# Kernel optimization log

Hardware: AMD Instinct MI355X
Metric: run time of the kernel (lower is better)

The kernel has to match this reference:

```python
import jax, jax.numpy as jnp
from jax import lax
import numpy as np

B, N, D = 8, 4096, 64
S = 1024          # groups
K = 32            # kneighbors
RADIUS = 0.2


def farthest_point_sample(xyz, npoint):
    """xyz: [B,N,3] -> centroid indices [B,npoint]. Deterministic start at index 0
    (original torch uses a random start index)."""
    b, n, _ = xyz.shape

    def step(carry, _):
        distance, farthest = carry                              # [B,N], [B]
        centroid = jnp.take_along_axis(xyz, farthest[:, None, None], axis=1)  # [B,1,3]
        dist = jnp.sum((xyz - centroid) ** 2, axis=-1)          # [B,N]
        distance = jnp.minimum(distance, dist)
        new_far = jnp.argmax(distance, axis=-1)
        return (distance, new_far), farthest

    init = (jnp.full((b, n), 1e10, xyz.dtype), jnp.zeros((b,), jnp.int32))
    _, cents = lax.scan(step, init, None, length=npoint)        # [npoint,B]
    return cents.T                                              # [B,npoint]


def square_distance(src, dst):
    # [B,N,M] squared euclidean distances
    d = -2.0 * jnp.einsum('bnc,bmc->bnm', src, dst)
    d += jnp.sum(src ** 2, -1)[:, :, None]
    d += jnp.sum(dst ** 2, -1)[:, None, :]
    return d


def query_ball_point(radius, nsample, xyz, new_xyz):
    b, n, _ = xyz.shape
    s = new_xyz.shape[1]
    sqrdists = square_distance(new_xyz, xyz)                    # [B,S,N]
    arange = jnp.arange(n, dtype=jnp.int32)[None, None, :]
    group_idx = jnp.where(sqrdists > radius ** 2, n, arange)    # [B,S,N]
    group_idx = jnp.sort(group_idx, axis=-1)[:, :, :nsample]    # [B,S,K]
    first = group_idx[:, :, :1]
    group_idx = jnp.where(group_idx == n, first, group_idx)
    return group_idx


def gather_points(points, idx):
    # points [B,N,C], idx [B,...] -> [B,...,C]
    return jax.vmap(lambda p, i: p[i])(points, idx)


def setup_inputs() -> dict:
    key = jax.random.key(0)
    k1, k2 = jax.random.split(key)
    xyz = jax.random.uniform(k1, (B, N, 3), dtype=jnp.float32)
    points = jax.random.normal(k2, (B, N, D), dtype=jnp.float32)
    return {"xyz": xyz, "points": points}


def reference(xyz, points):
    fps_idx = farthest_point_sample(xyz, S)                     # [B,S]
    new_xyz = gather_points(xyz, fps_idx)                       # [B,S,3]
    anchor_feat = gather_points(points, fps_idx)                # [B,S,D]
    idx = query_ball_point(RADIUS, K, xyz, new_xyz)             # [B,S,K]
    grouped_xyz = gather_points(xyz, idx)                       # [B,S,K,3]
    grouped_points = gather_points(points, idx)                 # [B,S,K,D]
    grouped_points = jnp.concatenate([grouped_points, grouped_xyz], axis=-1)  # use_xyz
    anchor_rep = jnp.broadcast_to(anchor_feat[:, :, None, :], (B, S, K, D))
    new_points = jnp.concatenate([grouped_points, anchor_rep], axis=-1)  # [B,S,K,2D+3]
    return new_xyz, new_points
```

## Files before the change

### kernel.cpp

```cpp
#include <hip/hip_runtime.h>

#define BB 8
#define NN 4096
#define DD 64
#define SS 1024
#define KK 32
#define R2 0.04f
#define NCONS_BLK 248
#define NCONS_WAVE (NCONS_BLK * 8)

typedef float f32x2 __attribute__((ext_vector_type(2)));

#define DPP_MAXF(wv, CTRL)                                                             \
    {                                                                                  \
        int _o = __builtin_amdgcn_update_dpp(__float_as_int(wv), __float_as_int(wv),   \
                                             CTRL, 0xf, 0xf, false);                   \
        (wv) = fmaxf((wv), __int_as_float(_o));                                        \
    }

__global__ __launch_bounds__(512) void fused_kernel(const float* __restrict__ xyz,
                                                    const float* __restrict__ points,
                                                    float* __restrict__ out,
                                                    int* __restrict__ fps_g,
                                                    int* __restrict__ progress) {
#pragma clang fp contract(off)
    __shared__ float4 sxyz[NN];
    __shared__ unsigned long long red[SS];
    __shared__ int sfar[SS];
    __shared__ int bbuf[8][KK];

    const int tid  = threadIdx.x;
    const int wave = tid >> 6;
    const int lane = tid & 63;

    if (blockIdx.x < BB) {
        const int b = blockIdx.x;
        const float* xb = xyz + (size_t)b * NN * 3;

        for (int i = tid; i < SS; i += 512) red[i] = 0ull;

        const float4* xb4 = (const float4*)(xb + tid * 24);
        const float4 q0 = xb4[0], q1 = xb4[1], q2 = xb4[2];
        const float4 q3 = xb4[3], q4 = xb4[4], q5 = xb4[5];

        f32x2 px[4], py[4], pz[4], dist[4];
        px[0] = (f32x2){q0.x, q0.w}; py[0] = (f32x2){q0.y, q1.x}; pz[0] = (f32x2){q0.z, q1.y};
        px[1] = (f32x2){q1.z, q2.y}; py[1] = (f32x2){q1.w, q2.z}; pz[1] = (f32x2){q2.x, q2.w};
        px[2] = (f32x2){q3.x, q3.w}; py[2] = (f32x2){q3.y, q4.x}; pz[2] = (f32x2){q3.z, q4.y};
        px[3] = (f32x2){q4.z, q5.y}; py[3] = (f32x2){q4.w, q5.z}; pz[3] = (f32x2){q5.x, q5.w};
#pragma unroll
        for (int jj = 0; jj < 4; ++jj) {
            const int i0 = tid * 8 + 2 * jj;
            sxyz[i0]     = make_float4(px[jj].x, py[jj].x, pz[jj].x, 0.0f);
            sxyz[i0 + 1] = make_float4(px[jj].y, py[jj].y, pz[jj].y, 0.0f);
            dist[jj] = (f32x2){1e10f, 1e10f};
        }
        __syncthreads();

        int far = 0;
        for (int t = 0; t < SS; ++t) {
            if (tid == 0) sfar[t] = far;
            const float4 c = sxyz[far];
            const f32x2 cx2 = (f32x2){c.x, c.x}, cy2 = (f32x2){c.y, c.y},
                        cz2 = (f32x2){c.z, c.z};

            f32x2 nd[4];
#pragma unroll
            for (int jj = 0; jj < 4; ++jj) {
                const f32x2 dx = px[jj] - cx2;
                const f32x2 dy = py[jj] - cy2;
                const f32x2 dz = pz[jj] - cz2;
                const f32x2 d  = (dx * dx + dy * dy) + dz * dz;
                f32x2 m;
                m.x = fminf(dist[jj].x, d.x);
                m.y = fminf(dist[jj].y, d.y);
                dist[jj] = m;
                nd[jj] = m;
            }
            const float bestv =
                fmaxf(fmaxf(fmaxf(nd[0].x, nd[0].y), fmaxf(nd[1].x, nd[1].y)),
                      fmaxf(fmaxf(nd[2].x, nd[2].y), fmaxf(nd[3].x, nd[3].y)));
            int localj = 0;
#pragma unroll
            for (int j = 7; j >= 0; --j) {
                const float v = (j & 1) ? nd[j >> 1].y : nd[j >> 1].x;
                if (v == bestv) localj = j;
            }

            float wv = bestv;
            DPP_MAXF(wv, 0x111);
            DPP_MAXF(wv, 0x112);
            DPP_MAXF(wv, 0x114);
            DPP_MAXF(wv, 0x118);
            DPP_MAXF(wv, 0x142);
            DPP_MAXF(wv, 0x143);
            const float maxw =
                __int_as_float(__builtin_amdgcn_readlane(__float_as_int(wv), 63));

            const unsigned long long hits = __ballot(bestv == maxw);
            const int L = __ffsll(hits) - 1;
            const int candv = tid * 8 + localj;
            const int cand  = __builtin_amdgcn_readlane(candv, L);

            if (lane == 0) {
                const unsigned long long p =
                    ((unsigned long long)__float_as_uint(maxw) << 32) | (unsigned)(~cand);
                atomicMax(&red[t], p);
            }
            __syncthreads();
            far = (int)(~(unsigned)red[t]);

            if ((t & 31) == 31 && wave == 7) {
                const int c0 = t - 31;
                if (lane < 32) fps_g[b * SS + c0 + lane] = sfar[c0 + lane];
                __threadfence();
                if (lane == 0)
                    __hip_atomic_store(&progress[b], t + 1, __ATOMIC_RELEASE,
                                       __HIP_MEMORY_SCOPE_AGENT);
            }
        }
    } else {
        const int wid = (blockIdx.x - BB) * 8 + wave;
        for (int g = wid; g < BB * SS; g += NCONS_WAVE) {
            const int b = g >> 10;
            const int s = g & (SS - 1);
            while (__hip_atomic_load(&progress[b], __ATOMIC_ACQUIRE,
                                     __HIP_MEMORY_SCOPE_AGENT) <= s)
                __builtin_amdgcn_s_sleep(32);
            const int qi = __hip_atomic_load(&fps_g[g], __ATOMIC_RELAXED,
                                             __HIP_MEMORY_SCOPE_AGENT);

            const float* xb = xyz + (size_t)b * NN * 3;
            const float* pb = points + (size_t)b * NN * DD;
            const float qx = xb[qi * 3 + 0], qy = xb[qi * 3 + 1], qz = xb[qi * 3 + 2];
            const float qn = __fadd_rn(__fadd_rn(__fmul_rn(qx, qx), __fmul_rn(qy, qy)),
                                       __fmul_rn(qz, qz));

            int total = 0;
            for (int base = 0; base < NN && total < KK; base += 64) {
                const int n  = base + lane;
                const float px = xb[n * 3 + 0], py = xb[n * 3 + 1], pz = xb[n * 3 + 2];
                const float pn = __fadd_rn(__fadd_rn(__fmul_rn(px, px), __fmul_rn(py, py)),
                                           __fmul_rn(pz, pz));
                const float dt = __fadd_rn(__fadd_rn(__fmul_rn(qx, px), __fmul_rn(qy, py)),
                                           __fmul_rn(qz, pz));
                const float d = __fadd_rn(__fadd_rn(__fmul_rn(-2.0f, dt), qn), pn);
                const bool hit = !(d > R2);
                const unsigned long long mask = __ballot(hit);
                const int before = __popcll(mask & ((1ull << lane) - 1ull));
                const int pos = total + before;
                if (hit && pos < KK) bbuf[wave][pos] = n;
                total += (int)__popcll(mask);
            }
            if (lane < KK) {
                const int v = (lane < total) ? bbuf[wave][lane] : bbuf[wave][0];
                bbuf[wave][lane] = v;
            }

            if (lane < 3) out[(size_t)g * 3 + lane] = xb[qi * 3 + lane];

            float* outp = out + (size_t)BB * SS * 3 + (size_t)g * (KK * 131);
            for (int c = lane; c < KK * 131; c += 64) {
                const int k = c / 131;
                const int j = c - k * 131;
                const int idx = bbuf[wave][k];
                float v;
                if (j < DD)          v = pb[idx * DD + j];
                else if (j < DD + 3) v = xb[idx * 3 + (j - DD)];
                else                 v = pb[qi * DD + (j - DD - 3)];
                outp[c] = v;
            }
        }
    }
}

extern "C" void kernel_launch(void* const* d_in, const int* in_sizes, int n_in,
                              void* d_out, int out_size, void* d_ws, size_t ws_size,
                              hipStream_t stream) {
    const float* xyz    = (const float*)d_in[0];
    const float* points = (const float*)d_in[1];
    float* out = (float*)d_out;

    int* fps_g    = (int*)d_ws;
    int* progress = fps_g + BB * SS;

    fused_kernel<<<BB + NCONS_BLK, 512, 0, stream>>>(xyz, points, out, fps_g, progress);
}
```

Before: 810.5 us.

## Replicate FPS per block and drop producer-consumer progress synchronization

The kernel now launches 32 blocks per batch. Every block recomputes the full farthest-point sampling for its batch and then groups its own slice of 32 centroids, reading coordinates from shared memory. This removes the global-memory progress flags, fences and spin-waiting between 8 producer blocks and many consumer blocks. The gather loop is also restructured so each lane writes one feature per neighbor. In exchange, the ball query and output writes no longer overlap with FPS; they run as a tail after it, and FPS work is duplicated 32 times. The padded shared array appears meant to keep one block per CU.

```diff
diff --git a/kernel.cpp b/kernel.cpp
--- a/kernel.cpp
+++ b/kernel.cpp
@@ -6,8 +6,6 @@
 #define SS 1024
 #define KK 32
 #define R2 0.04f
-#define NCONS_BLK 248
-#define NCONS_WAVE (NCONS_BLK * 8)
 
 typedef float f32x2 __attribute__((ext_vector_type(2)));
 
@@ -20,156 +18,142 @@
 
 __global__ __launch_bounds__(512) void fused_kernel(const float* __restrict__ xyz,
                                                     const float* __restrict__ points,
-                                                    float* __restrict__ out,
-                                                    int* __restrict__ fps_g,
-                                                    int* __restrict__ progress) {
+                                                    float* __restrict__ out) {
 #pragma clang fp contract(off)
     __shared__ float4 sxyz[NN];
-    __shared__ unsigned long long red[SS];
+    __shared__ unsigned long long red[SS + 416];
     __shared__ int sfar[SS];
     __shared__ int bbuf[8][KK];
 
     const int tid  = threadIdx.x;
     const int wave = tid >> 6;
     const int lane = tid & 63;
+    const int b    = blockIdx.x >> 5;
+    const int cs   = blockIdx.x & 31;
+    const float* xb = xyz + (size_t)b * NN * 3;
+    const float* pb = points + (size_t)b * NN * DD;
 
-    if (blockIdx.x < BB) {
-        const int b = blockIdx.x;
-        const float* xb = xyz + (size_t)b * NN * 3;
+    for (int i = tid; i < SS; i += 512) red[i] = 0ull;
 
-        for (int i = tid; i < SS; i += 512) red[i] = 0ull;
+    const float4* xb4 = (const float4*)(xb + tid * 24);
+    const float4 q0 = xb4[0], q1 = xb4[1], q2 = xb4[2];
+    const float4 q3 = xb4[3], q4 = xb4[4], q5 = xb4[5];
 
-        const float4* xb4 = (const float4*)(xb + tid * 24);
-        const float4 q0 = xb4[0], q1 = xb4[1], q2 = xb4[2];
-        const float4 q3 = xb4[3], q4 = xb4[4], q5 = xb4[5];
+    f32x2 px[4], py[4], pz[4], dist[4];
+    px[0] = (f32x2){q0.x, q0.w}; py[0] = (f32x2){q0.y, q1.x}; pz[0] = (f32x2){q0.z, q1.y};
+    px[1] = (f32x2){q1.z, q2.y}; py[1] = (f32x2){q1.w, q2.z}; pz[1] = (f32x2){q2.x, q2.w};
+    px[2] = (f32x2){q3.x, q3.w}; py[2] = (f32x2){q3.y, q4.x}; pz[2] = (f32x2){q3.z, q4.y};
+    px[3] = (f32x2){q4.z, q5.y}; py[3] = (f32x2){q4.w, q5.z}; pz[3] = (f32x2){q5.x, q5.w};
+#pragma unroll
+    for (int jj = 0; jj < 4; ++jj) {
+        const int i0 = tid * 8 + 2 * jj;
+        sxyz[i0]     = make_float4(px[jj].x, py[jj].x, pz[jj].x, 0.0f);
+        sxyz[i0 + 1] = make_float4(px[jj].y, py[jj].y, pz[jj].y, 0.0f);
+        dist[jj] = (f32x2){1e10f, 1e10f};
+    }
+    __syncthreads();
 
-        f32x2 px[4], py[4], pz[4], dist[4];
-        px[0] = (f32x2){q0.x, q0.w}; py[0] = (f32x2){q0.y, q1.x}; pz[0] = (f32x2){q0.z, q1.y};
-        px[1] = (f32x2){q1.z, q2.y}; py[1] = (f32x2){q1.w, q2.z}; pz[1] = (f32x2){q2.x, q2.w};
-        px[2] = (f32x2){q3.x, q3.w}; py[2] = (f32x2){q3.y, q4.x}; pz[2] = (f32x2){q3.z, q4.y};
-        px[3] = (f32x2){q4.z, q5.y}; py[3] = (f32x2){q4.w, q5.z}; pz[3] = (f32x2){q5.x, q5.w};
+    int far = 0;
+    for (int t = 0; t < SS; ++t) {
+        if (tid == 0) sfar[t] = far;
+        const float4 c = sxyz[far];
+        const f32x2 cx2 = (f32x2){c.x, c.x}, cy2 = (f32x2){c.y, c.y},
+                    cz2 = (f32x2){c.z, c.z};
+
+        f32x2 nd[4];
 #pragma unroll
         for (int jj = 0; jj < 4; ++jj) {
-            const int i0 = tid * 8 + 2 * jj;
-            sxyz[i0]     = make_float4(px[jj].x, py[jj].x, pz[jj].x, 0.0f);
-            sxyz[i0 + 1] = make_float4(px[jj].y, py[jj].y, pz[jj].y, 0.0f);
-            dist[jj] = (f32x2){1e10f, 1e10f};
+            const f32x2 dx = px[jj] - cx2;
+            const f32x2 dy = py[jj] - cy2;
+            const f32x2 dz = pz[jj] - cz2;
+            const f32x2 d  = (dx * dx + dy * dy) + dz * dz;
+            f32x2 m;
+            m.x = fminf(dist[jj].x, d.x);
+            m.y = fminf(dist[jj].y, d.y);
+            dist[jj] = m;
+            nd[jj] = m;
+        }
+        const float bestv =
+            fmaxf(fmaxf(fmaxf(nd[0].x, nd[0].y), fmaxf(nd[1].x, nd[1].y)),
+                  fmaxf(fmaxf(nd[2].x, nd[2].y), fmaxf(nd[3].x, nd[3].y)));
+        int localj = 0;
+#pragma unroll
+        for (int j = 7; j >= 0; --j) {
+            const float v = (j & 1) ? nd[j >> 1].y : nd[j >> 1].x;
+            if (v == bestv) localj = j;
+        }
+
+        float wv = bestv;
+        DPP_MAXF(wv, 0x111);
+        DPP_MAXF(wv, 0x112);
+        DPP_MAXF(wv, 0x114);
+        DPP_MAXF(wv, 0x118);
+        DPP_MAXF(wv, 0x142);
+        DPP_MAXF(wv, 0x143);
+        const float maxw =
+            __int_as_float(__builtin_amdgcn_readlane(__float_as_int(wv), 63));
+
+        const unsigned long long hits = __ballot(bestv == maxw);
+        const int L = __ffsll(hits) - 1;
+        const int candv = tid * 8 + localj;
+        const int cand  = __builtin_amdgcn_readlane(candv, L);
+
+        if (lane == 0) {
+            const unsigned long long p =
+                ((unsigned long long)__float_as_uint(maxw) << 32) | (unsigned)(~cand);
+            atomicMax(&red[t], p);
         }
         __syncthreads();
+        far = (int)(~(unsigned)red[t]);
+    }
 
-        int far = 0;
-        for (int t = 0; t < SS; ++t) {
-            if (tid == 0) sfar[t] = far;
-            const float4 c = sxyz[far];
-            const f32x2 cx2 = (f32x2){c.x, c.x}, cy2 = (f32x2){c.y, c.y},
-                        cz2 = (f32x2){c.z, c.z};
+#pragma unroll
+    for (int i = 0; i < 4; ++i) {
+        const int s  = cs * 32 + wave * 4 + i;
+        const int g  = b * SS + s;
+        const int qi = sfar[s];
+        const float4 q = sxyz[qi];
+        const float qn = __fadd_rn(__fadd_rn(__fmul_rn(q.x, q.x), __fmul_rn(q.y, q.y)),
+                                   __fmul_rn(q.z, q.z));
 
-            f32x2 nd[4];
-#pragma unroll
-            for (int jj = 0; jj < 4; ++jj) {
-                const f32x2 dx = px[jj] - cx2;
-                const f32x2 dy = py[jj] - cy2;
-                const f32x2 dz = pz[jj] - cz2;
-                const f32x2 d  = (dx * dx + dy * dy) + dz * dz;
-                f32x2 m;
-                m.x = fminf(dist[jj].x, d.x);
-                m.y = fminf(dist[jj].y, d.y);
-                dist[jj] = m;
-                nd[jj] = m;
-            }
-            const float bestv =
-                fmaxf(fmaxf(fmaxf(nd[0].x, nd[0].y), fmaxf(nd[1].x, nd[1].y)),
-                      fmaxf(fmaxf(nd[2].x, nd[2].y), fmaxf(nd[3].x, nd[3].y)));
-            int localj = 0;
-#pragma unroll
-            for (int j = 7; j >= 0; --j) {
-                const float v = (j & 1) ? nd[j >> 1].y : nd[j >> 1].x;
-                if (v == bestv) localj = j;
-            }
+        int total = 0;
+        for (int base = 0; base < NN && total < KK; base += 64) {
+            const int n = base + lane;
+            const float4 p = sxyz[n];
+            const float pn = __fadd_rn(__fadd_rn(__fmul_rn(p.x, p.x), __fmul_rn(p.y, p.y)),
+                                       __fmul_rn(p.z, p.z));
+            const float dt = __fadd_rn(__fadd_rn(__fmul_rn(q.x, p.x), __fmul_rn(q.y, p.y)),
+                                       __fmul_rn(q.z, p.z));
+            const float d = __fadd_rn(__fadd_rn(__fmul_rn(-2.0f, dt), qn), pn);
+            const bool hit = !(d > R2);
+            const unsigned long long mask = __ballot(hit);
+            const int before = __popcll(mask & ((1ull << lane) - 1ull));
+            const int pos = total + before;
+            if (hit && pos < KK) bbuf[wave][pos] = n;
+            total += (int)__popcll(mask);
+        }
+        if (lane < KK) {
+            const int v = (lane < total) ? bbuf[wave][lane] : bbuf[wave][0];
+            bbuf[wave][lane] = v;
+        }
 
-            float wv = bestv;
-            DPP_MAXF(wv, 0x111);
-            DPP_MAXF(wv, 0x112);
-            DPP_MAXF(wv, 0x114);
-            DPP_MAXF(wv, 0x118);
-            DPP_MAXF(wv, 0x142);
-            DPP_MAXF(wv, 0x143);
-            const float maxw =
-                __int_as_float(__builtin_amdgcn_readlane(__float_as_int(wv), 63));
+        if (lane < 3)
+            out[(size_t)g * 3 + lane] = (lane == 0) ? q.x : (lane == 1) ? q.y : q.z;
 
-            const unsigned long long hits = __ballot(bestv == maxw);
-            const int L = __ffsll(hits) - 1;
-            const int candv = tid * 8 + localj;
-            const int cand  = __builtin_amdgcn_readlane(candv, L);
+        const float a1 = (lane >= 3) ? pb[qi * DD + (lane - 3)] : 0.0f;
+        const float a2 = (lane < 3) ? pb[qi * DD + (61 + lane)] : 0.0f;
 
-            if (lane == 0) {
-                const unsigned long long p =
-                    ((unsigned long long)__float_as_uint(maxw) << 32) | (unsigned)(~cand);
-                atomicMax(&red[t], p);
-            }
-            __syncthreads();
-            far = (int)(~(unsigned)red[t]);
-
-            if ((t & 31) == 31 && wave == 7) {
-                const int c0 = t - 31;
-                if (lane < 32) fps_g[b * SS + c0 + lane] = sfar[c0 + lane];
-                __threadfence();
-                if (lane == 0)
-                    __hip_atomic_store(&progress[b], t + 1, __ATOMIC_RELEASE,
-                                       __HIP_MEMORY_SCOPE_AGENT);
-            }
-        }
-    } else {
-        const int wid = (blockIdx.x - BB) * 8 + wave;
-        for (int g = wid; g < BB * SS; g += NCONS_WAVE) {
-            const int b = g >> 10;
-            const int s = g & (SS - 1);
-            while (__hip_atomic_load(&progress[b], __ATOMIC_ACQUIRE,
-                                     __HIP_MEMORY_SCOPE_AGENT) <= s)
-                __builtin_amdgcn_s_sleep(32);
-            const int qi = __hip_atomic_load(&fps_g[g], __ATOMIC_RELAXED,
-                                             __HIP_MEMORY_SCOPE_AGENT);
-
-            const float* xb = xyz + (size_t)b * NN * 3;
-            const float* pb = points + (size_t)b * NN * DD;
-            const float qx = xb[qi * 3 + 0], qy = xb[qi * 3 + 1], qz = xb[qi * 3 + 2];
-            const float qn = __fadd_rn(__fadd_rn(__fmul_rn(qx, qx), __fmul_rn(qy, qy)),
-                                       __fmul_rn(qz, qz));
-
-            int total = 0;
-            for (int base = 0; base < NN && total < KK; base += 64) {
-                const int n  = base + lane;
-                const float px = xb[n * 3 + 0], py = xb[n * 3 + 1], pz = xb[n * 3 + 2];
-                const float pn = __fadd_rn(__fadd_rn(__fmul_rn(px, px), __fmul_rn(py, py)),
-                                           __fmul_rn(pz, pz));
-                const float dt = __fadd_rn(__fadd_rn(__fmul_rn(qx, px), __fmul_rn(qy, py)),
-                                           __fmul_rn(qz, pz));
-                const float d = __fadd_rn(__fadd_rn(__fmul_rn(-2.0f, dt), qn), pn);
-                const bool hit = !(d > R2);
-                const unsigned long long mask = __ballot(hit);
-                const int before = __popcll(mask & ((1ull << lane) - 1ull));
-                const int pos = total + before;
-                if (hit && pos < KK) bbuf[wave][pos] = n;
-                total += (int)__popcll(mask);
-            }
-            if (lane < KK) {
-                const int v = (lane < total) ? bbuf[wave][lane] : bbuf[wave][0];
-                bbuf[wave][lane] = v;
-            }
-
-            if (lane < 3) out[(size_t)g * 3 + lane] = xb[qi * 3 + lane];
-
-            float* outp = out + (size_t)BB * SS * 3 + (size_t)g * (KK * 131);
-            for (int c = lane; c < KK * 131; c += 64) {
-                const int k = c / 131;
-                const int j = c - k * 131;
-                const int idx = bbuf[wave][k];
-                float v;
-                if (j < DD)          v = pb[idx * DD + j];
-                else if (j < DD + 3) v = xb[idx * 3 + (j - DD)];
-                else                 v = pb[qi * DD + (j - DD - 3)];
-                outp[c] = v;
-            }
+        float* outp = out + (size_t)BB * SS * 3 + (size_t)g * (KK * 131);
+        for (int k = 0; k < KK; ++k) {
+            const int idx = bbuf[wave][k];
+            const float4 pi = sxyz[idx];
+            outp[k * 131 + lane] = pb[idx * DD + lane];
+            const float v1 = (lane == 0) ? pi.x
+                           : (lane == 1) ? pi.y
+                           : (lane == 2) ? pi.z
+                                         : a1;
+            outp[k * 131 + 64 + lane] = v1;
+            if (lane < 3) outp[k * 131 + 128 + lane] = a2;
         }
     }
 }
@@ -181,8 +165,5 @@
     const float* points = (const float*)d_in[1];
     float* out = (float*)d_out;
 
-    int* fps_g    = (int*)d_ws;
-    int* progress = fps_g + BB * SS;
-
-    fused_kernel<<<BB + NCONS_BLK, 512, 0, stream>>>(xyz, points, out, fps_g, progress);
+    fused_kernel<<<BB * 32, 512, 0, stream>>>(xyz, points, out);
 }
```

After: 739.2 us. 8.8% less time.
